# Optimization experiments

Measured on AMD Instinct MI355X. Metric: run time of the kernel, lower is better.

The kernel has to match this reference:

```python
import jax, jax.numpy as jnp
import numpy as np

N = 20000; E = 320000; G = 64; IN = 64; HID = 128; H = 8; HD = H * HID  # 1024


def setup_inputs() -> dict:
    key = jax.random.key(0)
    ks = jax.random.split(key, 32)
    inp = {}
    inp['x'] = jax.random.normal(ks[0], (N, IN), jnp.float32)
    inp['edge_index'] = jax.random.randint(ks[1], (2, E), 0, N, dtype=jnp.int64)
    inp['batch'] = jnp.sort(jax.random.randint(ks[2], (N,), 0, G, dtype=jnp.int64))
    dims_in = [IN, HD, HD]
    k = 3
    for i in range(3):
        d_in = dims_in[i]
        inp[f'gat_W{i}'] = jax.random.normal(ks[k], (d_in, HD), jnp.float32) * (1.0 / np.sqrt(d_in)); k += 1
        inp[f'gat_b{i}'] = jnp.zeros((HD,), jnp.float32)
        inp[f'att_src{i}'] = jax.random.normal(ks[k], (H, HID), jnp.float32) * 0.1; k += 1
        inp[f'att_dst{i}'] = jax.random.normal(ks[k], (H, HID), jnp.float32) * 0.1; k += 1
    for i in range(2):
        inp[f'boot_W{i}'] = jax.random.normal(ks[k], (HD, HD), jnp.float32) * (1.0 / np.sqrt(HD)); k += 1
        inp[f'boot_b{i}'] = jnp.zeros((HD,), jnp.float32)
    inp['clf_W1'] = jax.random.normal(ks[k], (HD, HID), jnp.float32) * (1.0 / np.sqrt(HD)); k += 1
    inp['clf_b1'] = jnp.zeros((HID,), jnp.float32)
    inp['clf_W2'] = jax.random.normal(ks[k], (HID, 2), jnp.float32) * (1.0 / np.sqrt(HID)); k += 1
    inp['clf_b2'] = jnp.zeros((2,), jnp.float32)
    return inp


def _gat_layer(x, W, b, a_src, a_dst, src, dst):
    # PyG GATConv (concat=True, self-loops already appended, eval mode => no dropout)
    h = (x @ W).reshape(N, H, HID)                      # [N,H,D]
    s = jnp.einsum('nhd,hd->nh', h, a_src)              # [N,H]
    t = jnp.einsum('nhd,hd->nh', h, a_dst)              # [N,H]
    e = jax.nn.leaky_relu(s[src] + t[dst], 0.2)         # [Etot,H]
    m = jax.ops.segment_max(e, dst, num_segments=N)     # segment softmax over incoming edges
    m = jnp.where(jnp.isfinite(m), m, 0.0)
    ex = jnp.exp(e - m[dst])
    denom = jax.ops.segment_sum(ex, dst, num_segments=N)
    alpha = ex / jnp.maximum(denom[dst], 1e-16)         # [Etot,H]
    out = jax.ops.segment_sum(alpha[:, :, None] * h[src], dst, num_segments=N)  # [N,H,D]
    return out.reshape(N, HD) + b


def reference(x, edge_index, batch,
              gat_W0, gat_b0, att_src0, att_dst0,
              gat_W1, gat_b1, att_src1, att_dst1,
              gat_W2, gat_b2, att_src2, att_dst2,
              boot_W0, boot_b0, boot_W1, boot_b1,
              clf_W1, clf_b1, clf_W2, clf_b2):
    loop = jnp.arange(N, dtype=edge_index.dtype)
    src = jnp.concatenate([edge_index[0], loop])
    dst = jnp.concatenate([edge_index[1], loop])
    gat = [(gat_W0, gat_b0, att_src0, att_dst0),
           (gat_W1, gat_b1, att_src1, att_dst1),
           (gat_W2, gat_b2, att_src2, att_dst2)]
    boot = [(boot_W0, boot_b0), (boot_W1, boot_b1)]
    h = x
    for i in range(3):
        W, b, a_s, a_d = gat[i]
        h = jax.nn.elu(_gat_layer(h, W, b, a_s, a_d, src, dst))
        if i < 2:
            noise = jax.random.normal(jax.random.key(100 + i), h.shape, h.dtype) * 0.1
            bW, bb = boot[i]
            h = (h + noise) @ bW + bb
    # global mean pool over graphs
    sums = jax.ops.segment_sum(h, batch, num_segments=G)        # [G,HD]
    cnts = jax.ops.segment_sum(jnp.ones((N,), h.dtype), batch, num_segments=G)
    g = sums / jnp.maximum(cnts, 1.0)[:, None]
    z = jax.nn.relu(g @ clf_W1 + clf_b1)                        # dropout = identity (eval)
    return z @ clf_W2 + clf_b2
```

## Files before the change

kernel.cpp:

```cpp
#include <hip/hip_runtime.h>
#include <stdint.h>

#define N_NODES 20000
#define N_EDGES 320000
#define E_TOT   (N_EDGES + N_NODES)
#define NGRAPH  64
#define DIN     64
#define DHID    128
#define NHEAD   8
#define HDIM    1024

typedef unsigned int u32;
typedef unsigned short u16;
typedef __bf16 bfx8 __attribute__((ext_vector_type(8)));
typedef float f32x4 __attribute__((ext_vector_type(4)));
typedef float f32x2 __attribute__((ext_vector_type(2)));

__device__ __forceinline__ u16 f2bf(float f){
  u32 u = __float_as_uint(f);
  u32 r = (u + 0x7FFFu + ((u >> 16) & 1u)) >> 16;
  return (u16)r;
}
__device__ __forceinline__ float bf2f(u16 v){
  return __uint_as_float(((u32)v) << 16);
}
__device__ __forceinline__ f32x2 up2(u32 u){
  f32x2 v;
  v.x = __uint_as_float(u << 16);
  v.y = __uint_as_float(u & 0xffff0000u);
  return v;
}

typedef __attribute__((address_space(3))) u32 lds_u32_t;
typedef const __attribute__((address_space(1))) u32 glb_u32_t;
__device__ __forceinline__ void g2l16(const void* g, void* l){
  __builtin_amdgcn_global_load_lds((glb_u32_t*)(uintptr_t)g,
                                   (lds_u32_t*)(uintptr_t)l, 16, 0, 0);
}

__device__ __forceinline__ u32 rotl32(u32 x, int r){ return (x<<r) | (x>>(32-r)); }

__device__ __forceinline__ void threefry2x32(u32 k0, u32 k1, u32 x0, u32 x1,
                                             u32& y0, u32& y1){
  u32 k2 = k0 ^ k1 ^ 0x1BD11BDAu;
  x0 += k0; x1 += k1;
#define TFR(r) { x0 += x1; x1 = rotl32(x1, (r)); x1 ^= x0; }
  TFR(13) TFR(15) TFR(26) TFR(6)
  x0 += k1; x1 += k2 + 1u;
  TFR(17) TFR(29) TFR(16) TFR(24)
  x0 += k2; x1 += k0 + 2u;
  TFR(13) TFR(15) TFR(26) TFR(6)
  x0 += k0; x1 += k1 + 3u;
  TFR(17) TFR(29) TFR(16) TFR(24)
  x0 += k1; x1 += k2 + 4u;
  TFR(13) TFR(15) TFR(26) TFR(6)
  x0 += k2; x1 += k0 + 5u;
#undef TFR
  y0 = x0; y1 = x1;
}

__device__ __forceinline__ float erfinv_fast(float x){
  float t = fmaf(-x, x, 1.0f);
  float w = -__logf(t);
  float p;
  if (w < 5.0f){
    w -= 2.5f;
    p = 2.81022636e-08f;
    p = fmaf(p, w, 3.43273939e-07f);
    p = fmaf(p, w, -3.5233877e-06f);
    p = fmaf(p, w, -4.39150654e-06f);
    p = fmaf(p, w, 0.00021858087f);
    p = fmaf(p, w, -0.00125372503f);
    p = fmaf(p, w, -0.00417768164f);
    p = fmaf(p, w, 0.246640727f);
    p = fmaf(p, w, 1.50140941f);
  } else {
    w = sqrtf(w) - 3.0f;
    p = -0.000200214257f;
    p = fmaf(p, w, 0.000100950558f);
    p = fmaf(p, w, 0.00134934322f);
    p = fmaf(p, w, -0.00367342844f);
    p = fmaf(p, w, 0.00573950773f);
    p = fmaf(p, w, -0.0076224613f);
    p = fmaf(p, w, 0.00943887047f);
    p = fmaf(p, w, 1.00167406f);
    p = fmaf(p, w, 2.83297682f);
  }
  return p * x;
}

__device__ __forceinline__ float jax_normal(u32 seed, u32 i){
  u32 y0, y1;
  threefry2x32(0u, seed, 0u, i, y0, y1);
  u32 bits = y0 ^ y1;
  float f = __uint_as_float((bits >> 9) | 0x3f800000u) - 1.0f;
  float xx = fmaxf(-0.99999994f, fmaf(f, 2.0f, -0.99999994f));
  return 1.41421356f * erfinv_fast(xx);
}

__global__ __launch_bounds__(256) void prep_misc_kernel(const float* __restrict__ x,
    const float* __restrict__ W0, const float* __restrict__ W1,
    u16* __restrict__ xbf, u16* __restrict__ O0, u16* __restrict__ O1,
    const int* __restrict__ ei, const int* __restrict__ batch,
    int* __restrict__ cnt, int* __restrict__ gcnt,
    const float* __restrict__ gatW0, const float* __restrict__ asrc0,
    const float* __restrict__ adst0, float* __restrict__ wst){
  const int z = blockIdx.y;
  if (z < 3){
    const float* S = (z==0) ? W0 : (z==1) ? W1 : x;
    u16* D = (z==0) ? O0 : (z==1) ? O1 : xbf;
    const int total = (z==2) ? N_NODES*DIN : HDIM*HDIM;
    int i = (blockIdx.x*256 + threadIdx.x)*4;
    if (i < total){
      float4 v = *(const float4*)(S + i);
      D[i+0] = f2bf(v.x); D[i+1] = f2bf(v.y);
      D[i+2] = f2bf(v.z); D[i+3] = f2bf(v.w);
    }
  } else if (z == 3){
    int i = blockIdx.x*256 + threadIdx.x;
    if (i < N_EDGES) atomicAdd(&cnt[ei[N_EDGES + i]], 1);
    else if (i < E_TOT) atomicAdd(&gcnt[batch[i - N_EDGES]], 1);
  } else {
    if (blockIdx.x == 0){
      for (int o = threadIdx.x; o < DIN*16; o += 256){
        const int d = o >> 4, c = o & 15;
        const int hh = c & 7;
        const float* av = ((c < 8) ? asrc0 : adst0) + hh*DHID;
        const float* wr = gatW0 + (size_t)d*HDIM + hh*DHID;
        float a = 0.f;
        for (int k = 0; k < DHID; ++k) a = fmaf(wr[k], av[k], a);
        wst[o] = a;
      }
    }
  }
}

__global__ __launch_bounds__(256) void st0_kernel(const float* __restrict__ x,
    const float* __restrict__ wst, float* __restrict__ sbuf,
    float* __restrict__ tbuf){
  const int n = blockIdx.x*256 + threadIdx.x;
  if (n >= N_NODES) return;
  float acc[16];
#pragma unroll
  for (int c = 0; c < 16; ++c) acc[c] = 0.f;
  const float* xr = x + (size_t)n*DIN;
  for (int d = 0; d < DIN; d += 4){
    const float4 xv = *(const float4*)(xr + d);
    const float* w0 = wst + d*16;
#pragma unroll
    for (int c = 0; c < 16; ++c){
      acc[c] = fmaf(xv.x, w0[c],      acc[c]);
      acc[c] = fmaf(xv.y, w0[16+c],   acc[c]);
      acc[c] = fmaf(xv.z, w0[32+c],   acc[c]);
      acc[c] = fmaf(xv.w, w0[48+c],   acc[c]);
    }
  }
#pragma unroll
  for (int h = 0; h < NHEAD; ++h){
    sbuf[n*NHEAD + h] = acc[h];
    tbuf[n*NHEAD + h] = acc[8 + h];
  }
}

__global__ __launch_bounds__(256) void transpose_all_kernel(
    const float* __restrict__ W0, const float* __restrict__ W1,
    const float* __restrict__ W2,
    u16* __restrict__ T0, u16* __restrict__ T1, u16* __restrict__ T2){
  const int z = blockIdx.z;
  const float* W = (z==0)?W0:(z==1)?W1:W2;
  u16* T = (z==0)?T0:(z==1)?T1:T2;
  const int K = (z==0)?DIN:HDIM;
  const int bk = blockIdx.y*32;
  if (bk >= K) return;
  __shared__ float t[32][33];
  int bn = blockIdx.x*32;
  int lx = threadIdx.x & 31, ly = threadIdx.x >> 5;
#pragma unroll
  for (int r = 0; r < 32; r += 8)
    t[ly+r][lx] = W[(size_t)(bk+ly+r)*HDIM + bn + lx];
  __syncthreads();
#pragma unroll
  for (int r = 0; r < 32; r += 8){
    const u16 v = f2bf(t[lx][ly+r]);
    if (z == 0){
      const size_t base = (size_t)(bn+ly+r)*128 + bk + lx;
      T[base] = v; T[base + 64] = v;
    } else {
      T[(size_t)(bn+ly+r)*K + bk + lx] = v;
    }
  }
}

__global__ __launch_bounds__(1024) void scan_pair_kernel(const int* __restrict__ cnt,
    int* __restrict__ rowptr, int* __restrict__ cursor, int* __restrict__ colidx,
    const int* __restrict__ gcnt, int* __restrict__ goff){
  if (blockIdx.x == 1){
    if (threadIdx.x == 0){
      int s = 0;
      for (int g = 0; g < NGRAPH; ++g){ goff[g] = s; s += gcnt[g]; }
      goff[NGRAPH] = s;
    }
    return;
  }
  __shared__ int wsum[16];
  __shared__ int carry_s;
  const int tid = threadIdx.x, lane = tid & 63, wv = tid >> 6;
  if (tid == 0){ carry_s = 0; rowptr[0] = 0; }
  __syncthreads();
  for (int base = 0; base < N_NODES; base += 1024){
    int i = base + tid;
    int v = (i < N_NODES) ? cnt[i] + 1 : 0;
    int s = v;
#pragma unroll
    for (int off = 1; off < 64; off <<= 1){
      int t = __shfl_up(s, off);
      if (lane >= off) s += t;
    }
    if (lane == 63) wsum[wv] = s;
    __syncthreads();
    if (wv == 0 && lane < 16){
      int ws = wsum[lane];
#pragma unroll
      for (int off = 1; off < 16; off <<= 1){
        int t = __shfl_up(ws, off);
        if (lane >= off) ws += t;
      }
      wsum[lane] = ws;
    }
    __syncthreads();
    int incl = s + ((wv > 0) ? wsum[wv-1] : 0) + carry_s;
    if (i < N_NODES){
      rowptr[i+1] = incl;
      const int slot = incl - v;
      colidx[slot] = i;
      cursor[i] = slot + 1;
    }
    __syncthreads();
    if (tid == 1023) carry_s = incl;
    __syncthreads();
  }
}

__global__ __launch_bounds__(256) void fill_edges_kernel(const int* __restrict__ ei,
    int* __restrict__ cursor, int* __restrict__ colidx){
  int e = blockIdx.x*256 + threadIdx.x;
  if (e < N_EDGES){
    int s = ei[e], d = ei[N_EDGES + e];
    int p = atomicAdd(&cursor[d], 1);
    colidx[p] = s;
  }
}

__device__ __forceinline__ void gemm_tile(const u16* __restrict__ A,
    const u16* __restrict__ BT, const float* __restrict__ bias,
    u16* __restrict__ Cb, int M, int K, int bm, int bn,
    u16* As, u16* Bs,
    const float* __restrict__ asrc, const float* __restrict__ adst,
    float* __restrict__ sbuf, float* __restrict__ tbuf,
    const int emode, const u32 seed){
  const int tid = threadIdx.x;
  const int lane = tid & 63, w = tid >> 6;
  const int wm = (w & 1)*64, wn = (w >> 1)*64;

  const int cid0 = tid, cid1 = 256 + tid;
  const int r0 = cid0 & 127, kc0 = cid0 >> 7;
  const int r1 = cid1 & 127, kc1 = cid1 >> 7;
  int ar0 = bm + r0; if (ar0 >= M) ar0 = M - 1;
  int ar1 = bm + r1; if (ar1 >= M) ar1 = M - 1;
  const u16* ag0 = A + (size_t)ar0*K + kc0*8;
  const u16* ag1 = A + (size_t)ar1*K + kc1*8;
  const u16* bg0 = BT + (size_t)(bn + r0)*K + kc0*8;
  const u16* bg1 = BT + (size_t)(bn + r1)*K + kc1*8;
  u16* al0 = As + cid0*8;  u16* al1 = As + cid1*8;
  u16* bl0 = Bs + cid0*8;  u16* bl1 = Bs + cid1*8;

  const int rowl = lane & 15, kg = lane >> 4;
  const bfx8* ap = (const bfx8*)(As + ((size_t)kg*128 + wm + rowl)*8);
  const bfx8* bp = (const bfx8*)(Bs + ((size_t)kg*128 + wn + rowl)*8);

  f32x4 acc[4][4] = {};
  for (int k0 = 0; k0 < K; k0 += 32){
    g2l16(ag0 + k0, al0);
    g2l16(ag1 + k0, al1);
    g2l16(bg0 + k0, bl0);
    g2l16(bg1 + k0, bl1);
    __syncthreads();
    bfx8 af[4], bfr[4];
#pragma unroll
    for (int i = 0; i < 4; ++i){ af[i] = ap[i*16]; bfr[i] = bp[i*16]; }
#pragma unroll
    for (int i = 0; i < 4; ++i)
#pragma unroll
      for (int j = 0; j < 4; ++j)
        acc[j][i] = __builtin_amdgcn_mfma_f32_16x16x32_bf16(bfr[j], af[i], acc[j][i], 0, 0, 0);
    __syncthreads();
  }

  const int quad = lane >> 4;
  const bool dost = (sbuf != nullptr);
  const int head = bn >> 7;
  float sl[4] = {0.f,0.f,0.f,0.f}, tl[4] = {0.f,0.f,0.f,0.f};
#pragma unroll
  for (int j = 0; j < 4; ++j){
    const int col0 = bn + wn + j*16 + quad*4;
    float4 bv = make_float4(0.f,0.f,0.f,0.f);
    if (bias) bv = *(const float4*)(bias + col0);
    float4 av = make_float4(0.f,0.f,0.f,0.f), dv = av;
    if (dost){
      const int d0 = col0 - bn;
      av = *(const float4*)(asrc + head*DHID + d0);
      dv = *(const float4*)(adst + head*DHID + d0);
    }
#pragma unroll
    for (int i = 0; i < 4; ++i){
      const int row = bm + wm + i*16 + rowl;
      if (emode == 1){
        if (row < M){
          float v0 = acc[j][i][0] + bv.x;
          float v1 = acc[j][i][1] + bv.y;
          float v2 = acc[j][i][2] + bv.z;
          float v3 = acc[j][i][3] + bv.w;
          v0 = (v0 > 0.f) ? v0 : __expf(v0) - 1.0f;
          v1 = (v1 > 0.f) ? v1 : __expf(v1) - 1.0f;
          v2 = (v2 > 0.f) ? v2 : __expf(v2) - 1.0f;
          v3 = (v3 > 0.f) ? v3 : __expf(v3) - 1.0f;
          const u32 ib = (u32)row*HDIM + (u32)col0;
          v0 = fmaf(0.1f, jax_normal(seed, ib+0u), v0);
          v1 = fmaf(0.1f, jax_normal(seed, ib+1u), v1);
          v2 = fmaf(0.1f, jax_normal(seed, ib+2u), v2);
          v3 = fmaf(0.1f, jax_normal(seed, ib+3u), v3);
          uint2 pk;
          pk.x = (u32)f2bf(v0) | ((u32)f2bf(v1) << 16);
          pk.y = (u32)f2bf(v2) | ((u32)f2bf(v3) << 16);
          *(uint2*)(Cb + (size_t)row*HDIM + col0) = pk;
        }
      } else {
        const u16 p0 = f2bf(acc[j][i][0] + bv.x);
        const u16 p1 = f2bf(acc[j][i][1] + bv.y);
        const u16 p2 = f2bf(acc[j][i][2] + bv.z);
        const u16 p3 = f2bf(acc[j][i][3] + bv.w);
        if (row < M){
          uint2 pk;
          pk.x = (u32)p0 | ((u32)p1 << 16);
          pk.y = (u32)p2 | ((u32)p3 << 16);
          *(uint2*)(Cb + (size_t)row*HDIM + col0) = pk;
        }
        if (dost){
          const float c0 = bf2f(p0), c1 = bf2f(p1), c2 = bf2f(p2), c3 = bf2f(p3);
          sl[i] = fmaf(c0, av.x, fmaf(c1, av.y, fmaf(c2, av.z, fmaf(c3, av.w, sl[i]))));
          tl[i] = fmaf(c0, dv.x, fmaf(c1, dv.y, fmaf(c2, dv.z, fmaf(c3, dv.w, tl[i]))));
        }
      }
    }
  }
  if (dost){
#pragma unroll
    for (int i = 0; i < 4; ++i){
      sl[i] += __shfl_xor(sl[i], 16); sl[i] += __shfl_xor(sl[i], 32);
      tl[i] += __shfl_xor(tl[i], 16); tl[i] += __shfl_xor(tl[i], 32);
    }
    float* sred = (float*)As;
    float* tred = sred + 128;
    if ((w >> 1) == 0 && quad == 0){
#pragma unroll
      for (int i = 0; i < 4; ++i){
        const int rl = wm + i*16 + rowl;
        sred[rl] = sl[i]; tred[rl] = tl[i];
      }
    }
    __syncthreads();
    if ((w >> 1) == 1 && quad == 0){
#pragma unroll
      for (int i = 0; i < 4; ++i){
        const int rl = wm + i*16 + rowl;
        const int row = bm + rl;
        if (row < M){
          sbuf[row*NHEAD + head] = sred[rl] + sl[i];
          tbuf[row*NHEAD + head] = tred[rl] + tl[i];
        }
      }
    }
  }
}

__global__ __launch_bounds__(256) void gemm_bf16(
    const u16* __restrict__ A, const u16* __restrict__ BT,
    const float* __restrict__ bias, u16* __restrict__ Cb, int M, int K,
    const float* __restrict__ asrc, const float* __restrict__ adst,
    float* __restrict__ sbuf, float* __restrict__ tbuf){
  __shared__ __align__(16) u16 As[4*128*8];
  __shared__ __align__(16) u16 Bs[4*128*8];
  const int kblk = blockIdx.y*8 + blockIdx.x;
  const int xc = kblk & 7, bq = (kblk >> 3) & 7, gq = kblk >> 6;
  const int bmi = gq*8 + xc;
  const int mt = (M + 127) >> 7;
  if (bmi >= mt) return;
  gemm_tile(A, BT, bias, Cb, M, K, bmi*128, bq*128, As, Bs,
            asrc, adst, sbuf, tbuf, 0, 0u);
}

__global__ __launch_bounds__(256) void gemm_l0t(
    const u16* __restrict__ agg2, const u16* __restrict__ BT,
    const float* __restrict__ bias, u16* __restrict__ Cb, u32 seed){
  __shared__ __align__(16) u16 As[4*128*8];
  __shared__ __align__(16) u16 Bs[4*128*8];
  const int head = blockIdx.x;
  const int bm = blockIdx.y*128;
  gemm_tile(agg2 + (size_t)head*N_NODES*128, BT, bias, Cb, N_NODES, 128,
            bm, head*128, As, Bs, nullptr, nullptr, nullptr, nullptr,
            1, seed);
}

__global__ __launch_bounds__(256) void wf_bias_kernel(
    const u16* __restrict__ A0, const u16* __restrict__ B0, u16* __restrict__ C0,
    const u16* __restrict__ A1, const u16* __restrict__ B1, u16* __restrict__ C1,
    const float* __restrict__ bb0, const u16* __restrict__ gwt0,
    const float* __restrict__ bb1, const u16* __restrict__ gwt1,
    float* __restrict__ fb0, float* __restrict__ fb1){
  __shared__ __align__(16) u16 As[4*128*8];
  __shared__ __align__(16) u16 Bs[4*128*8];
  if (blockIdx.z < 2){
    const u16* A = blockIdx.z ? A1 : A0;
    const u16* B = blockIdx.z ? B1 : B0;
    u16* C = blockIdx.z ? C1 : C0;
    gemm_tile(A, B, nullptr, C, HDIM, HDIM, blockIdx.y*128, blockIdx.x*128,
              As, Bs, nullptr, nullptr, nullptr, nullptr, 0, 0u);
  } else {
    const int kb = blockIdx.y*8 + blockIdx.x;
    const int wv = threadIdx.x >> 6, lane = threadIdx.x & 63;
    for (int idx = kb*4 + wv; idx < 2*HDIM; idx += 256){
      const int set = idx >> 10, n = idx & (HDIM-1);
      const float* bb = set ? bb1 : bb0;
      const u16* row = (set ? gwt1 : gwt0) + (size_t)n*HDIM + lane*16;
      const float* bp = bb + lane*16;
      float acc = 0.f;
#pragma unroll
      for (int k = 0; k < 16; ++k) acc = fmaf(bp[k], bf2f(row[k]), acc);
      for (int off = 32; off > 0; off >>= 1) acc += __shfl_down(acc, off);
      if (lane == 0) (set ? fb1 : fb0)[n] = acc;
    }
  }
}

__global__ __launch_bounds__(256) void gat_agg_kernel(const u16* __restrict__ hlin,
    const float* __restrict__ sbuf, const float* __restrict__ tbuf,
    const int* __restrict__ rowptr, const int* __restrict__ colidx,
    const float* __restrict__ bias, float* __restrict__ outf,
    u16* __restrict__ outbf, u32 seed){
  const int tid  = threadIdx.x;
  const int lane = tid & 63;
  const int n    = blockIdx.x*4 + (tid >> 6);
  const int jsub = lane >> 3;
  const int hh   = lane & 7;
  const int hA   = lane >> 3;
  const int row0 = rowptr[n];
  const int deg  = rowptr[n+1] - row0;
  const float tn = tbuf[n*NHEAD + hh];
  const char* hl = (const char*)hlin;
  const u32 lb   = (u32)lane << 5;

  f32x2 acc[8] = {};
  float m_run = -INFINITY, d_run = 0.f;

  for (int c = 0; c < deg; c += 8){
    const int ne = min(8, deg - c);
    const int jj = (jsub < ne) ? jsub : (ne - 1);
    const int srcv = colidx[row0 + c + jj];
    float e = sbuf[srcv*NHEAD + hh] + tn;
    e = (e > 0.f) ? e : 0.2f*e;
    if (jsub >= ne) e = -INFINITY;
    float mc = e;
    mc = fmaxf(mc, __shfl_xor(mc, 8));
    mc = fmaxf(mc, __shfl_xor(mc, 16));
    mc = fmaxf(mc, __shfl_xor(mc, 32));
    const float mnew = fmaxf(m_run, mc);
    const float w = __expf(e - mnew);
    float ws = w;
    ws += __shfl_xor(ws, 8);
    ws += __shfl_xor(ws, 16);
    ws += __shfl_xor(ws, 32);
    const float r = (m_run == -INFINITY) ? 0.0f : __expf(m_run - mnew);
    d_run = fmaf(d_run, r, ws);
    m_run = mnew;
    const float rA = __shfl(r, hA);
    const f32x2 r2 = {rA, rA};
#pragma unroll
    for (int q = 0; q < 8; ++q) acc[q] *= r2;
    int j = 0;
    for (; j + 2 <= ne; j += 2){
      const int s0 = __builtin_amdgcn_readlane(srcv, j*8);
      const int s1 = __builtin_amdgcn_readlane(srcv, j*8 + 8);
      const float w0 = __shfl(w, j*8 + hA);
      const float w1 = __shfl(w, j*8 + 8 + hA);
      const char* rp0 = hl + (((size_t)(u32)s0) << 11);
      const char* rp1 = hl + (((size_t)(u32)s1) << 11);
      const uint4 a0 = *(const uint4*)(rp0 + lb);
      const uint4 a1 = *(const uint4*)(rp0 + lb + 16);
      const uint4 b0 = *(const uint4*)(rp1 + lb);
      const uint4 b1 = *(const uint4*)(rp1 + lb + 16);
      const f32x2 w02 = {w0, w0}, w12 = {w1, w1};
      acc[0] = __builtin_elementwise_fma(w02, up2(a0.x), acc[0]);
      acc[1] = __builtin_elementwise_fma(w02, up2(a0.y), acc[1]);
      acc[2] = __builtin_elementwise_fma(w02, up2(a0.z), acc[2]);
      acc[3] = __builtin_elementwise_fma(w02, up2(a0.w), acc[3]);
      acc[4] = __builtin_elementwise_fma(w02, up2(a1.x), acc[4]);
      acc[5] = __builtin_elementwise_fma(w02, up2(a1.y), acc[5]);
      acc[6] = __builtin_elementwise_fma(w02, up2(a1.z), acc[6]);
      acc[7] = __builtin_elementwise_fma(w02, up2(a1.w), acc[7]);
      acc[0] = __builtin_elementwise_fma(w12, up2(b0.x), acc[0]);
      acc[1] = __builtin_elementwise_fma(w12, up2(b0.y), acc[1]);
      acc[2] = __builtin_elementwise_fma(w12, up2(b0.z), acc[2]);
      acc[3] = __builtin_elementwise_fma(w12, up2(b0.w), acc[3]);
      acc[4] = __builtin_elementwise_fma(w12, up2(b1.x), acc[4]);
      acc[5] = __builtin_elementwise_fma(w12, up2(b1.y), acc[5]);
      acc[6] = __builtin_elementwise_fma(w12, up2(b1.z), acc[6]);
      acc[7] = __builtin_elementwise_fma(w12, up2(b1.w), acc[7]);
    }
    if (j < ne){
      const int s0 = __builtin_amdgcn_readlane(srcv, j*8);
      const float w0 = __shfl(w, j*8 + hA);
      const char* rp0 = hl + (((size_t)(u32)s0) << 11);
      const uint4 a0 = *(const uint4*)(rp0 + lb);
      const uint4 a1 = *(const uint4*)(rp0 + lb + 16);
      const f32x2 w02 = {w0, w0};
      acc[0] = __builtin_elementwise_fma(w02, up2(a0.x), acc[0]);
      acc[1] = __builtin_elementwise_fma(w02, up2(a0.y), acc[1]);
      acc[2] = __builtin_elementwise_fma(w02, up2(a0.z), acc[2]);
      acc[3] = __builtin_elementwise_fma(w02, up2(a0.w), acc[3]);
      acc[4] = __builtin_elementwise_fma(w02, up2(a1.x), acc[4]);
      acc[5] = __builtin_elementwise_fma(w02, up2(a1.y), acc[5]);
      acc[6] = __builtin_elementwise_fma(w02, up2(a1.z), acc[6]);
      acc[7] = __builtin_elementwise_fma(w02, up2(a1.w), acc[7]);
    }
  }

  const float dA = __shfl(d_run, hA);
  const float invA = 1.0f / fmaxf(dA, 1e-16f);
  float o[16];
#pragma unroll
  for (int q = 0; q < 8; ++q){ o[2*q] = acc[q].x; o[2*q+1] = acc[q].y; }
  const float4* bp = (const float4*)(bias + lane*16);
#pragma unroll
  for (int q = 0; q < 4; ++q){
    const float4 bv = bp[q];
    o[4*q+0] = fmaf(o[4*q+0], invA, bv.x);
    o[4*q+1] = fmaf(o[4*q+1], invA, bv.y);
    o[4*q+2] = fmaf(o[4*q+2], invA, bv.z);
    o[4*q+3] = fmaf(o[4*q+3], invA, bv.w);
  }
#pragma unroll
  for (int k = 0; k < 16; ++k)
    o[k] = (o[k] > 0.f) ? o[k] : __expf(o[k]) - 1.0f;
  if (outbf){
    const u32 ib = (u32)n*HDIM + (u32)lane*16u;
    u32 pk[8];
#pragma unroll
    for (int q = 0; q < 8; ++q){
      const float v0 = fmaf(0.1f, jax_normal(seed, ib + 2u*q + 0u), o[2*q+0]);
      const float v1 = fmaf(0.1f, jax_normal(seed, ib + 2u*q + 1u), o[2*q+1]);
      pk[q] = (u32)f2bf(v0) | ((u32)f2bf(v1) << 16);
    }
    uint4* dst = (uint4*)(outbf + (size_t)n*HDIM + lane*16);
    dst[0] = make_uint4(pk[0], pk[1], pk[2], pk[3]);
    dst[1] = make_uint4(pk[4], pk[5], pk[6], pk[7]);
  } else {
    float4* dst = (float4*)(outf + (size_t)n*HDIM + lane*16);
#pragma unroll
    for (int q = 0; q < 4; ++q)
      dst[q] = make_float4(o[4*q], o[4*q+1], o[4*q+2], o[4*q+3]);
  }
}

__global__ __launch_bounds__(256) void agg_x_kernel(const u16* __restrict__ xbf,
    const float* __restrict__ sbuf, const float* __restrict__ tbuf,
    const int* __restrict__ rowptr, const int* __restrict__ colidx,
    u16* __restrict__ agg2){
  const int tid  = threadIdx.x;
  const int lane = tid & 63;
  const int n    = blockIdx.x*4 + (tid >> 6);
  const int jsub = lane >> 3;
  const int hh   = lane & 7;
  const int hA   = lane >> 3;
  const int row0 = rowptr[n];
  const int deg  = rowptr[n+1] - row0;
  const float tn = tbuf[n*NHEAD + hh];
  const char* xb = (const char*)xbf;
  const u32 lb   = (u32)(lane & 7) << 4;

  f32x2 acc[4] = {};
  float m_run = -INFINITY, d_run = 0.f;

  for (int c = 0; c < deg; c += 8){
    const int ne = min(8, deg - c);
    const int jj = (jsub < ne) ? jsub : (ne - 1);
    const int srcv = colidx[row0 + c + jj];
    float e = sbuf[srcv*NHEAD + hh] + tn;
    e = (e > 0.f) ? e : 0.2f*e;
    if (jsub >= ne) e = -INFINITY;
    float mc = e;
    mc = fmaxf(mc, __shfl_xor(mc, 8));
    mc = fmaxf(mc, __shfl_xor(mc, 16));
    mc = fmaxf(mc, __shfl_xor(mc, 32));
    const float mnew = fmaxf(m_run, mc);
    const float w = __expf(e - mnew);
    float ws = w;
    ws += __shfl_xor(ws, 8);
    ws += __shfl_xor(ws, 16);
    ws += __shfl_xor(ws, 32);
    const float r = (m_run == -INFINITY) ? 0.0f : __expf(m_run - mnew);
    d_run = fmaf(d_run, r, ws);
    m_run = mnew;
    const float rA = __shfl(r, hA);
    const f32x2 r2 = {rA, rA};
#pragma unroll
    for (int q = 0; q < 4; ++q) acc[q] *= r2;
    int j = 0;
    for (; j + 2 <= ne; j += 2){
      const int s0 = __builtin_amdgcn_readlane(srcv, j*8);
      const int s1 = __builtin_amdgcn_readlane(srcv, j*8 + 8);
      const float w0 = __shfl(w, j*8 + hA);
      const float w1 = __shfl(w, j*8 + 8 + hA);
      const uint4 a0 = *(const uint4*)(xb + (((size_t)(u32)s0) << 7) + lb);
      const uint4 b0 = *(const uint4*)(xb + (((size_t)(u32)s1) << 7) + lb);
      const f32x2 w02 = {w0, w0}, w12 = {w1, w1};
      acc[0] = __builtin_elementwise_fma(w02, up2(a0.x), acc[0]);
      acc[1] = __builtin_elementwise_fma(w02, up2(a0.y), acc[1]);
      acc[2] = __builtin_elementwise_fma(w02, up2(a0.z), acc[2]);
      acc[3] = __builtin_elementwise_fma(w02, up2(a0.w), acc[3]);
      acc[0] = __builtin_elementwise_fma(w12, up2(b0.x), acc[0]);
      acc[1] = __builtin_elementwise_fma(w12, up2(b0.y), acc[1]);
      acc[2] = __builtin_elementwise_fma(w12, up2(b0.z), acc[2]);
      acc[3] = __builtin_elementwise_fma(w12, up2(b0.w), acc[3]);
    }
    if (j < ne){
      const int s0 = __builtin_amdgcn_readlane(srcv, j*8);
      const float w0 = __shfl(w, j*8 + hA);
      const uint4 a0 = *(const uint4*)(xb + (((size_t)(u32)s0) << 7) + lb);
      const f32x2 w02 = {w0, w0};
      acc[0] = __builtin_elementwise_fma(w02, up2(a0.x), acc[0]);
      acc[1] = __builtin_elementwise_fma(w02, up2(a0.y), acc[1]);
      acc[2] = __builtin_elementwise_fma(w02, up2(a0.z), acc[2]);
      acc[3] = __builtin_elementwise_fma(w02, up2(a0.w), acc[3]);
    }
  }

  const float dA = __shfl(d_run, hA);
  const float invA = 1.0f / fmaxf(dA, 1e-16f);
  float v[8];
#pragma unroll
  for (int q = 0; q < 4; ++q){ v[2*q] = acc[q].x*invA; v[2*q+1] = acc[q].y*invA; }
  u32 hp[4], lp[4];
#pragma unroll
  for (int q = 0; q < 4; ++q){
    const u16 h0 = f2bf(v[2*q]),   h1 = f2bf(v[2*q+1]);
    const u16 l0 = f2bf(v[2*q]   - bf2f(h0));
    const u16 l1 = f2bf(v[2*q+1] - bf2f(h1));
    hp[q] = (u32)h0 | ((u32)h1 << 16);
    lp[q] = (u32)l0 | ((u32)l1 << 16);
  }
  u16* base = agg2 + ((size_t)hA*N_NODES + (size_t)n)*128 + (lane & 7)*8;
  *(uint4*)(base)      = make_uint4(hp[0], hp[1], hp[2], hp[3]);
  *(uint4*)(base + 64) = make_uint4(lp[0], lp[1], lp[2], lp[3]);
}

__global__ __launch_bounds__(256) void pool_sum_kernel(const float* __restrict__ h,
    const int* __restrict__ batch, float* __restrict__ gsum){
  const int n0 = blockIdx.x*128;
  const int n1 = min(n0 + 128, N_NODES);
  const int cb = threadIdx.x*4;
  float4 acc = make_float4(0.f,0.f,0.f,0.f);
  int curg = batch[n0];
  for (int n = n0; n < n1; ++n){
    const int g = batch[n];
    if (g != curg){
      atomicAdd(&gsum[curg*HDIM + cb+0], acc.x);
      atomicAdd(&gsum[curg*HDIM + cb+1], acc.y);
      atomicAdd(&gsum[curg*HDIM + cb+2], acc.z);
      atomicAdd(&gsum[curg*HDIM + cb+3], acc.w);
      acc = make_float4(0.f,0.f,0.f,0.f);
      curg = g;
    }
    const float4 v = *(const float4*)(h + (size_t)n*HDIM + cb);
    acc.x += v.x; acc.y += v.y; acc.z += v.z; acc.w += v.w;
  }
  atomicAdd(&gsum[curg*HDIM + cb+0], acc.x);
  atomicAdd(&gsum[curg*HDIM + cb+1], acc.y);
  atomicAdd(&gsum[curg*HDIM + cb+2], acc.z);
  atomicAdd(&gsum[curg*HDIM + cb+3], acc.w);
}

__global__ __launch_bounds__(256) void pool_clf_kernel(const float* __restrict__ gsum,
    const int* __restrict__ gcnt,
    const float* __restrict__ W1, const float* __restrict__ b1,
    const float* __restrict__ W2, const float* __restrict__ b2,
    float* __restrict__ out){
  __shared__ float gs[HDIM];
  __shared__ float z[DHID];
  const int g = blockIdx.x, tid = threadIdx.x;
  const int cb = tid*4;
  const float invc = 1.0f / fmaxf((float)gcnt[g], 1.0f);
  const float4 s = *(const float4*)(gsum + (size_t)g*HDIM + cb);
  gs[cb+0] = s.x*invc; gs[cb+1] = s.y*invc;
  gs[cb+2] = s.z*invc; gs[cb+3] = s.w*invc;
  __syncthreads();
  if (tid < DHID){
    float a = b1[tid];
    for (int k = 0; k < HDIM; ++k) a = fmaf(gs[k], W1[k*DHID + tid], a);
    z[tid] = fmaxf(a, 0.0f);
  }
  __syncthreads();
  if (tid < 2){
    float o = b2[tid];
    for (int k = 0; k < DHID; ++k) o = fmaf(z[k], W2[k*2 + tid], o);
    out[g*2 + tid] = o;
  }
}

extern "C" void kernel_launch(void* const* d_in, const int* in_sizes, int n_in,
                              void* d_out, int out_size, void* d_ws, size_t ws_size,
                              hipStream_t stream){
  const float* x      = (const float*)d_in[0];
  const int*   ei     = (const int*)d_in[1];
  const int*   batch  = (const int*)d_in[2];
  const float* gatW[3]  = {(const float*)d_in[3],  (const float*)d_in[7],  (const float*)d_in[11]};
  const float* gatB[3]  = {(const float*)d_in[4],  (const float*)d_in[8],  (const float*)d_in[12]};
  const float* asrc[3]  = {(const float*)d_in[5],  (const float*)d_in[9],  (const float*)d_in[13]};
  const float* adst[3]  = {(const float*)d_in[6],  (const float*)d_in[10], (const float*)d_in[14]};
  const float* bootW[2] = {(const float*)d_in[15], (const float*)d_in[17]};
  const float* bootB[2] = {(const float*)d_in[16], (const float*)d_in[18]};
  const float* clfW1 = (const float*)d_in[19];
  const float* clfb1 = (const float*)d_in[20];
  const float* clfW2 = (const float*)d_in[21];
  const float* clfb2 = (const float*)d_in[22];
  float* outp = (float*)d_out;

  float* fws  = (float*)d_ws;
  float* hB   = fws;
  float* sbuf = hB + (size_t)N_NODES*HDIM;
  float* tbuf = sbuf + (size_t)N_NODES*NHEAD;
  float* fbias0 = tbuf + (size_t)N_NODES*NHEAD;
  float* fbias1 = fbias0 + HDIM;
  u16* xbf    = (u16*)(fbias1 + HDIM);
  u16* hAbf   = xbf + (size_t)N_NODES*DIN;
  u16* hBbf   = hAbf + (size_t)N_NODES*HDIM;
  u16* wt[3];
  wt[0] = hBbf + (size_t)N_NODES*HDIM;
  wt[1] = wt[0] + (size_t)HDIM*128;
  wt[2] = wt[1] + (size_t)HDIM*HDIM;
  u16* wnt0   = wt[2] + (size_t)HDIM*HDIM;
  u16* wnt1   = wnt0 + (size_t)HDIM*HDIM;
  u16* wf0    = wnt1 + (size_t)HDIM*HDIM;
  u16* wf1    = wf0 + (size_t)HDIM*HDIM;
  int* rowptr = (int*)(wf1 + (size_t)HDIM*HDIM);
  int* cursor = rowptr + (N_NODES+1);
  int* colidx = cursor + N_NODES;
  int* gcnt   = colidx + E_TOT;
  int* cnt    = gcnt + NGRAPH;
  float* gsum = (float*)(cnt + N_NODES);
  int* goff   = (int*)(gsum + (size_t)NGRAPH*HDIM);
  float* wst  = (float*)(goff + NGRAPH + 1);

  u16* agg2 = hAbf;

  (void)hipMemsetAsync(gcnt, 0, (NGRAPH + N_NODES + NGRAPH*HDIM)*sizeof(int), stream);

  const int nb_e = (N_EDGES + 255)/256;

  prep_misc_kernel<<<dim3((E_TOT + 255)/256, 5), 256, 0, stream>>>(
      x, bootW[0], bootW[1], xbf, wnt0, wnt1, ei, batch, cnt, gcnt,
      gatW[0], asrc[0], adst[0], wst);
  st0_kernel<<<(N_NODES + 255)/256, 256, 0, stream>>>(x, wst, sbuf, tbuf);
  transpose_all_kernel<<<dim3(HDIM/32, HDIM/32, 3), 256, 0, stream>>>(
      gatW[0], gatW[1], gatW[2], wt[0], wt[1], wt[2]);
  scan_pair_kernel<<<2, 1024, 0, stream>>>(cnt, rowptr, cursor, colidx, gcnt, goff);
  fill_edges_kernel<<<nb_e, 256, 0, stream>>>(ei, cursor, colidx);

  wf_bias_kernel<<<dim3(8, 8, 3), 256, 0, stream>>>(
      wt[1], wnt0, wf0, wt[2], wnt1, wf1,
      bootB[0], wt[1], bootB[1], wt[2], fbias0, fbias1);

  const int mt = (N_NODES + 127)/128;
  dim3 gemmGrid(8, (mt + 7)/8*8);

  agg_x_kernel<<<N_NODES/4, 256, 0, stream>>>(xbf, sbuf, tbuf, rowptr, colidx,
                                              agg2);
  gemm_l0t<<<dim3(8, mt), 256, 0, stream>>>(agg2, wt[0], gatB[0], hBbf, 100u);

  gemm_bf16<<<gemmGrid, 256, 0, stream>>>(hBbf, wf0, fbias0, hAbf, N_NODES, HDIM,
                                          asrc[1], adst[1], sbuf, tbuf);
  gat_agg_kernel<<<N_NODES/4, 256, 0, stream>>>(hAbf, sbuf, tbuf, rowptr, colidx,
                                                gatB[1], nullptr, hBbf, 101u);
  gemm_bf16<<<gemmGrid, 256, 0, stream>>>(hBbf, wf1, fbias1, hAbf, N_NODES, HDIM,
                                          asrc[2], adst[2], sbuf, tbuf);
  gat_agg_kernel<<<N_NODES/4, 256, 0, stream>>>(hAbf, sbuf, tbuf, rowptr, colidx,
                                                gatB[2], hB, nullptr, 0u);

  pool_sum_kernel<<<(N_NODES + 127)/128, 256, 0, stream>>>(hB, batch, gsum);
  pool_clf_kernel<<<NGRAPH, 256, 0, stream>>>(gsum, gcnt,
                                              clfW1, clfb1, clfW2, clfb2, outp);
}
```

Before: 870.0 us.

## Fuse global mean-pool summation into final GAT aggregation kernel

The last GAT aggregation kernel no longer writes the full fp32 node-feature matrix. It reduces its four nodes per block in shared memory and atomically adds the result straight into the per-graph sums, and the separate pool_sum kernel is removed. This avoids an ~80 MB write and re-read of node features plus one launch. In exchange it issues many more global float atomics to a small set of addresses, which can contend. It also adds a 16 KB shared buffer that the earlier-layer launch of the same kernel carries too, which may lower occupancy.

```diff
diff --git a/kernel.cpp b/kernel.cpp
--- a/kernel.cpp
+++ b/kernel.cpp
@@ -445,11 +445,14 @@
 __global__ __launch_bounds__(256) void gat_agg_kernel(const u16* __restrict__ hlin,
     const float* __restrict__ sbuf, const float* __restrict__ tbuf,
     const int* __restrict__ rowptr, const int* __restrict__ colidx,
-    const float* __restrict__ bias, float* __restrict__ outf,
+    const float* __restrict__ bias,
+    const int* __restrict__ batch, float* __restrict__ gsum,
     u16* __restrict__ outbf, u32 seed){
+  __shared__ float red[4][HDIM];
   const int tid  = threadIdx.x;
   const int lane = tid & 63;
-  const int n    = blockIdx.x*4 + (tid >> 6);
+  const int wv   = tid >> 6;
+  const int n    = blockIdx.x*4 + wv;
   const int jsub = lane >> 3;
   const int hh   = lane & 7;
   const int hA   = lane >> 3;
@@ -564,10 +567,29 @@
     dst[0] = make_uint4(pk[0], pk[1], pk[2], pk[3]);
     dst[1] = make_uint4(pk[4], pk[5], pk[6], pk[7]);
   } else {
-    float4* dst = (float4*)(outf + (size_t)n*HDIM + lane*16);
+    float* rw = &red[wv][lane*16];
 #pragma unroll
     for (int q = 0; q < 4; ++q)
-      dst[q] = make_float4(o[4*q], o[4*q+1], o[4*q+2], o[4*q+3]);
+      *(float4*)(rw + q*4) = make_float4(o[4*q], o[4*q+1], o[4*q+2], o[4*q+3]);
+    __syncthreads();
+    const int g0 = batch[blockIdx.x*4];
+    const int g3 = batch[blockIdx.x*4 + 3];
+    if (g0 == g3){
+      const int d = tid*4;
+      float4 s;
+      s.x = red[0][d+0] + red[1][d+0] + red[2][d+0] + red[3][d+0];
+      s.y = red[0][d+1] + red[1][d+1] + red[2][d+1] + red[3][d+1];
+      s.z = red[0][d+2] + red[1][d+2] + red[2][d+2] + red[3][d+2];
+      s.w = red[0][d+3] + red[1][d+3] + red[2][d+3] + red[3][d+3];
+      float* gp = gsum + (size_t)g0*HDIM + d;
+      atomicAdd(gp+0, s.x); atomicAdd(gp+1, s.y);
+      atomicAdd(gp+2, s.z); atomicAdd(gp+3, s.w);
+    } else {
+      const int gn = batch[n];
+      float* gp = gsum + (size_t)gn*HDIM + lane*16;
+#pragma unroll
+      for (int k = 0; k < 16; ++k) atomicAdd(gp + k, o[k]);
+    }
   }
 }
 
@@ -661,32 +683,6 @@
   u16* base = agg2 + ((size_t)hA*N_NODES + (size_t)n)*128 + (lane & 7)*8;
   *(uint4*)(base)      = make_uint4(hp[0], hp[1], hp[2], hp[3]);
   *(uint4*)(base + 64) = make_uint4(lp[0], lp[1], lp[2], lp[3]);
-}
-
-__global__ __launch_bounds__(256) void pool_sum_kernel(const float* __restrict__ h,
-    const int* __restrict__ batch, float* __restrict__ gsum){
-  const int n0 = blockIdx.x*128;
-  const int n1 = min(n0 + 128, N_NODES);
-  const int cb = threadIdx.x*4;
-  float4 acc = make_float4(0.f,0.f,0.f,0.f);
-  int curg = batch[n0];
-  for (int n = n0; n < n1; ++n){
-    const int g = batch[n];
-    if (g != curg){
-      atomicAdd(&gsum[curg*HDIM + cb+0], acc.x);
-      atomicAdd(&gsum[curg*HDIM + cb+1], acc.y);
-      atomicAdd(&gsum[curg*HDIM + cb+2], acc.z);
-      atomicAdd(&gsum[curg*HDIM + cb+3], acc.w);
-      acc = make_float4(0.f,0.f,0.f,0.f);
-      curg = g;
-    }
-    const float4 v = *(const float4*)(h + (size_t)n*HDIM + cb);
-    acc.x += v.x; acc.y += v.y; acc.z += v.z; acc.w += v.w;
-  }
-  atomicAdd(&gsum[curg*HDIM + cb+0], acc.x);
-  atomicAdd(&gsum[curg*HDIM + cb+1], acc.y);
-  atomicAdd(&gsum[curg*HDIM + cb+2], acc.z);
-  atomicAdd(&gsum[curg*HDIM + cb+3], acc.w);
 }
 
 __global__ __launch_bounds__(256) void pool_clf_kernel(const float* __restrict__ gsum,
@@ -789,13 +785,12 @@
   gemm_bf16<<<gemmGrid, 256, 0, stream>>>(hBbf, wf0, fbias0, hAbf, N_NODES, HDIM,
                                           asrc[1], adst[1], sbuf, tbuf);
   gat_agg_kernel<<<N_NODES/4, 256, 0, stream>>>(hAbf, sbuf, tbuf, rowptr, colidx,
-                                                gatB[1], nullptr, hBbf, 101u);
+                                                gatB[1], batch, gsum, hBbf, 101u);
   gemm_bf16<<<gemmGrid, 256, 0, stream>>>(hBbf, wf1, fbias1, hAbf, N_NODES, HDIM,
                                           asrc[2], adst[2], sbuf, tbuf);
   gat_agg_kernel<<<N_NODES/4, 256, 0, stream>>>(hAbf, sbuf, tbuf, rowptr, colidx,
-                                                gatB[2], hB, nullptr, 0u);
-
-  pool_sum_kernel<<<(N_NODES + 127)/128, 256, 0, stream>>>(hB, batch, gsum);
+                                                gatB[2], batch, gsum, nullptr, 0u);
+
   pool_clf_kernel<<<NGRAPH, 256, 0, stream>>>(gsum, gcnt,
                                               clfW1, clfb1, clfW2, clfb2, outp);
 }
```

Result: faster. 832.8 us (-4.3%).
